# Optimization experiments

Measured on AMD Instinct MI355X. Metric: run time of the kernel, lower is better.

Reference implementation:

```python
import jax, jax.numpy as jnp
import numpy as np
from jax import lax

D_MODEL = 1024
D_STATE = 16
D_CONV = 4
EXPAND = 2
D_INNER = EXPAND * D_MODEL          # 2048
DT_RANK = (D_MODEL + 15) // 16      # 64


def setup_inputs() -> dict:
    key = jax.random.key(0)
    ks = jax.random.split(key, 12)
    B, L = 2, 2048
    s = lambda *sh: 1.0 / np.sqrt(sh[-1])
    inp = {
        "x": jax.random.normal(ks[0], (B, L, D_MODEL), jnp.float32),
        "in_proj_w": jax.random.normal(ks[1], (2 * D_INNER, D_MODEL), jnp.float32) * s(0, D_MODEL),
        "conv_w": jax.random.normal(ks[2], (D_INNER, 1, D_CONV), jnp.float32) * s(0, D_CONV),
        "conv_b": jax.random.normal(ks[3], (D_INNER,), jnp.float32) * 0.01,
        "x_proj_w": jax.random.normal(ks[4], (DT_RANK + 2 * D_STATE, D_INNER), jnp.float32) * s(0, D_INNER),
        "dt_proj_w": jax.random.normal(ks[5], (D_INNER, DT_RANK), jnp.float32) * s(0, DT_RANK),
        "dt_proj_b": jax.random.normal(ks[6], (D_INNER,), jnp.float32) * 0.1 - 4.0,  # softplus(dt) small
        "A_log": jnp.log(jnp.broadcast_to(jnp.arange(1, D_STATE + 1, dtype=jnp.float32), (D_INNER, D_STATE))),
        "D": jnp.ones((D_INNER,), jnp.float32),
        "out_proj_w": jax.random.normal(ks[7], (D_MODEL, D_INNER), jnp.float32) * s(0, D_INNER),
        "ln_w": jnp.ones((D_MODEL,), jnp.float32),
        "ln_b": jnp.zeros((D_MODEL,), jnp.float32),
    }
    return inp


def _mamba(x, in_proj_w, conv_w, conv_b, x_proj_w, dt_proj_w, dt_proj_b, A_log, D, out_proj_w):
    B, L, _ = x.shape
    xz = jnp.einsum("bld,ed->ble", x, in_proj_w)          # [B,L,2*d_inner]
    xi, z = jnp.split(xz, 2, axis=-1)                       # each [B,L,d_inner]

    # causal depthwise conv1d over time
    xt = jnp.transpose(xi, (0, 2, 1))                       # [B,d_inner,L]
    xc = lax.conv_general_dilated(
        xt, conv_w, window_strides=(1,), padding=[(D_CONV - 1, 0)],
        dimension_numbers=("NCH", "OIH", "NCH"), feature_group_count=D_INNER)
    xc = jax.nn.silu(xc + conv_b[None, :, None])            # [B,d_inner,L]
    u = jnp.transpose(xc, (0, 2, 1))                        # [B,L,d_inner]

    x_dbl = jnp.einsum("bld,ed->ble", u, x_proj_w)          # [B,L,dt_rank+2N]
    dt, Bm, Cm = jnp.split(x_dbl, [DT_RANK, DT_RANK + D_STATE], axis=-1)
    delta = jax.nn.softplus(jnp.einsum("blr,dr->bld", dt, dt_proj_w) + dt_proj_b)  # [B,L,d_inner]

    A = -jnp.exp(A_log)                                     # [d_inner,N]

    def step(h, inputs):
        d_t, B_t, C_t, u_t = inputs                         # [B,d], [B,N], [B,N], [B,d]
        dA = jnp.exp(d_t[..., None] * A)                    # [B,d_inner,N]
        h = dA * h + (d_t * u_t)[..., None] * B_t[:, None, :]
        y_t = jnp.einsum("bdn,bn->bd", h, C_t)
        return h, y_t

    xs = (jnp.transpose(delta, (1, 0, 2)), jnp.transpose(Bm, (1, 0, 2)),
          jnp.transpose(Cm, (1, 0, 2)), jnp.transpose(u, (1, 0, 2)))
    h0 = jnp.zeros((B, D_INNER, D_STATE), x.dtype)
    _, ys = lax.scan(step, h0, xs)                          # ys [L,B,d_inner]
    y = jnp.transpose(ys, (1, 0, 2)) + u * D                # skip connection
    y = y * jax.nn.silu(z)                                  # gate
    return jnp.einsum("bld,ed->ble", y, out_proj_w)         # [B,L,d_model]


def reference(x, in_proj_w, conv_w, conv_b, x_proj_w, dt_proj_w, dt_proj_b,
              A_log, D, out_proj_w, ln_w, ln_b):
    residual = x
    y = _mamba(x, in_proj_w, conv_w, conv_b, x_proj_w, dt_proj_w, dt_proj_b,
               A_log, D, out_proj_w)
    # dropout is identity in eval; residual + LayerNorm
    h = y + residual
    mu = jnp.mean(h, axis=-1, keepdims=True)
    var = jnp.var(h, axis=-1, keepdims=True)
    return (h - mu) * lax.rsqrt(var + 1e-5) * ln_w + ln_b
```

## Files before the change

kernel.cpp:

```cpp
#include <hip/hip_runtime.h>

typedef unsigned short u16;
typedef __attribute__((ext_vector_type(8))) short bf8_t;
typedef __attribute__((ext_vector_type(4))) float f4_t;
typedef __attribute__((ext_vector_type(4))) unsigned short u16x4;
typedef __attribute__((ext_vector_type(8))) unsigned short u16x8;

__device__ __forceinline__ float b2f(u16 h) {
  union { unsigned u; float f; } v; v.u = ((unsigned)h) << 16; return v.f;
}
__device__ __forceinline__ u16 f2b(float f) {
  union { float f; unsigned u; } v; v.f = f;
  unsigned u = v.u;
  u += 0x7fffu + ((u >> 16) & 1u);
  return (u16)(u >> 16);
}

#define AS1C(p) ((const __attribute__((address_space(1))) void*)(p))
#define AS3(p)  ((__attribute__((address_space(3))) void*)(p))

__global__ __launch_bounds__(256)
void cvt_all(const float* __restrict__ x, const float* __restrict__ inW,
             const float* __restrict__ xprojW, const float* __restrict__ dtW,
             const float* __restrict__ outW,
             u16* __restrict__ xb, u16* __restrict__ inWb, u16* __restrict__ xpb,
             u16* __restrict__ dtWb, u16* __restrict__ outWb)
{
  int i = blockIdx.x * 256 + threadIdx.x;
  if (i >= 2703360) return;
  const float* s; u16* d; int off;
  if (i < 1048576)      { s = x;      d = xb;    off = i; }
  else if (i < 2097152) { s = inW;    d = inWb;  off = i - 1048576; }
  else if (i < 2146304) { s = xprojW; d = xpb;   off = i - 2097152; }
  else if (i < 2179072) { s = dtW;    d = dtWb;  off = i - 2146304; }
  else                  { s = outW;   d = outWb; off = i - 2179072; }
  f4_t v = *(const f4_t*)(s + (size_t)off * 4);
  u16x4 o;
#pragma unroll
  for (int j = 0; j < 4; ++j) o[j] = f2b(v[j]);
  *(u16x4*)(d + (size_t)off * 4) = o;
}

__device__ __forceinline__ void stage64(const u16* g, int ld, int row0, int rowmax,
                                        int k0, u16* lds, int wid, int lane) {
  int qg = (lane & 7) ^ ((lane >> 3) & 7);
#pragma unroll
  for (int c = 0; c < 4; ++c) {
    int chunk = wid * 4 + c;
    int r = row0 + chunk * 8 + (lane >> 3);
    if (r > rowmax) r = rowmax;
    const u16* gp = g + (size_t)r * ld + k0 + qg * 8;
    __builtin_amdgcn_global_load_lds(AS1C(gp), AS3(lds + chunk * 512), 16, 0, 0);
  }
}

template<int EPI>
__device__ __forceinline__ void gemm_body(const u16* __restrict__ A, int lda,
             const u16* __restrict__ Bt, int ldb,
             int Kblk, int Nact,
             u16* __restrict__ o16, float* __restrict__ of32,
             float* __restrict__ of32b, const float* __restrict__ biasf)
{
  __shared__ u16 lsA[128 * 64];
  __shared__ u16 lsB[128 * 64];
  const int tid = threadIdx.x;
  const int wid = tid >> 6, lane = tid & 63;
  const int wm = wid >> 1, wn = wid & 1;
  const int lrow = lane & 15;
  const int kq = lane >> 4;
  const int sw = lrow & 7;
  const int m0 = blockIdx.y * 128;
  const int n0 = (EPI == 1) ? 0 : blockIdx.x * 128;
  int kbase = 0;
  if (EPI == 1) kbase = blockIdx.x * Kblk;

  f4_t acc[4][4];
#pragma unroll
  for (int i = 0; i < 4; ++i)
#pragma unroll
    for (int j = 0; j < 4; ++j) acc[i][j] = {0.f, 0.f, 0.f, 0.f};

  for (int kt = kbase; kt < kbase + Kblk; kt += 64) {
    stage64(A,  lda, m0, 0x3fffffff, kt, lsA, wid, lane);
    stage64(Bt, ldb, n0, Nact - 1,   kt, lsB, wid, lane);
    __syncthreads();
#pragma unroll
    for (int h = 0; h < 2; ++h) {
      const int lk = ((h * 4 + kq) ^ sw) * 8;
      bf8_t af[4], bfr[4];
#pragma unroll
      for (int mi = 0; mi < 4; ++mi)
        af[mi] = *(const bf8_t*)&lsA[(wm * 64 + mi * 16 + lrow) * 64 + lk];
#pragma unroll
      for (int ni = 0; ni < 4; ++ni)
        bfr[ni] = *(const bf8_t*)&lsB[(wn * 64 + ni * 16 + lrow) * 64 + lk];
#pragma unroll
      for (int mi = 0; mi < 4; ++mi)
#pragma unroll
        for (int ni = 0; ni < 4; ++ni)
          acc[mi][ni] = __builtin_amdgcn_mfma_f32_16x16x32_bf16(af[mi], bfr[ni], acc[mi][ni], 0, 0, 0);
    }
    __syncthreads();
  }

  const int rq = (lane >> 4) * 4;
#pragma unroll
  for (int mi = 0; mi < 4; ++mi) {
#pragma unroll
    for (int ni = 0; ni < 4; ++ni) {
#pragma unroll
      for (int r = 0; r < 4; ++r) {
        int m = m0 + wm * 64 + mi * 16 + rq + r;
        int n = n0 + wn * 64 + ni * 16 + lrow;
        float v = acc[mi][ni][r];
        if (EPI == 1) {
          if (n < 96) of32[((size_t)blockIdx.x * 4096 + m) * 96 + n] = v;
        } else if (EPI == 2) {
          float t = v + biasf[n];
          float sp = (t > 20.f) ? t : log1pf(__expf(t));
          o16[(size_t)m * 2048 + n] = f2b(sp);
        }
      }
    }
  }
}

__global__ __launch_bounds__(256)
void gemm_xp(const u16* A, int lda, const u16* Bt, int ldb, int Kblk, int Nact,
             u16* o16, float* of32, float* of32b, const float* biasf)
{ gemm_body<1>(A, lda, Bt, ldb, Kblk, Nact, o16, of32, of32b, biasf); }

__global__ __launch_bounds__(256)
void gemm_dt(const u16* A, int lda, const u16* Bt, int ldb, int Kblk, int Nact,
             u16* o16, float* of32, float* of32b, const float* biasf)
{ gemm_body<2>(A, lda, Bt, ldb, Kblk, Nact, o16, of32, of32b, biasf); }


__device__ __forceinline__ void stageu(const u16* __restrict__ g, int ld,
                                       int row0, int k0, u16* ldsu,
                                       int wid, int lane) {
  int qg = (lane & 7) ^ ((lane >> 3) & 7);
#pragma unroll
  for (int j = 0; j < 2; ++j) {
    int rr = j * 64 + wid * 8 + (lane >> 3);
    const u16* gp = g + (size_t)(row0 + rr) * ld + k0 + qg * 8;
    __builtin_amdgcn_global_load_lds(AS1C(gp), AS3(ldsu + (j * 512 + wid * 64) * 8), 16, 0, 0);
  }
}

#define G8_BAR()   __builtin_amdgcn_s_barrier()
#define G8_LGKM0() do { asm volatile("s_waitcnt lgkmcnt(0)" ::: "memory"); \
                        __builtin_amdgcn_sched_barrier(0); } while (0)
#define G8_LGKM8() asm volatile("s_waitcnt lgkmcnt(8)" ::: "memory")
#define G8_VM(N)   do { asm volatile("s_waitcnt vmcnt(" #N ")" ::: "memory"); \
                        __builtin_amdgcn_sched_barrier(0); } while (0)

#define RD_A(base, MH) do { \
  _Pragma("unroll") \
  for (int mi_ = 0; mi_ < 4; ++mi_) { \
    af[mi_][0] = *(const bf8_t*)((base) + arow + ((MH) * 64 + mi_ * 16) * 64 + aq0); \
    af[mi_][1] = *(const bf8_t*)((base) + arow + ((MH) * 64 + mi_ * 16) * 64 + aq1); \
  } } while (0)

#define RD_B(base, NH) do { \
  _Pragma("unroll") \
  for (int ni_ = 0; ni_ < 2; ++ni_) { \
    bfr[NH][ni_][0] = *(const bf8_t*)((base) + brow + ((NH) * 32 + ni_ * 16) * 64 + aq0); \
    bfr[NH][ni_][1] = *(const bf8_t*)((base) + brow + ((NH) * 32 + ni_ * 16) * 64 + aq1); \
  } } while (0)

#define MMA(MH, NH) do { \
  __builtin_amdgcn_s_setprio(1); \
  _Pragma("unroll") \
  for (int mi_ = 0; mi_ < 4; ++mi_) \
    _Pragma("unroll") \
    for (int ni_ = 0; ni_ < 2; ++ni_) { \
      acc[(MH) * 4 + mi_][(NH) * 2 + ni_] = __builtin_amdgcn_mfma_f32_16x16x32_bf16( \
          af[mi_][0], bfr[NH][ni_][0], acc[(MH) * 4 + mi_][(NH) * 2 + ni_], 0, 0, 0); \
      acc[(MH) * 4 + mi_][(NH) * 2 + ni_] = __builtin_amdgcn_mfma_f32_16x16x32_bf16( \
          af[mi_][1], bfr[NH][ni_][1], acc[(MH) * 4 + mi_][(NH) * 2 + ni_], 0, 0, 0); \
    } \
  __builtin_amdgcn_s_setprio(0); \
} while (0)

__global__ __launch_bounds__(512, 2)
void gemm8_in(const u16* __restrict__ A, const u16* __restrict__ Bt,
              u16* __restrict__ o16)
{
  __shared__ u16 ls[65536];
  const int tid = threadIdx.x;
  const int wid = tid >> 6, lane = tid & 63;
  const int wm = wid >> 2, wn = wid & 3;
  const int lrow = lane & 15;
  const int kq = lane >> 4;
  const int sw = lrow & 7;
  const int m0 = blockIdx.y * 256;
  const int n0 = blockIdx.x * 256;
  u16* lsA0 = ls;
  u16* lsB0 = ls + 16384;
  u16* lsA1 = ls + 32768;
  u16* lsB1 = ls + 49152;
  const int arow = (wm * 128 + lrow) * 64;
  const int brow = (wn * 64 + lrow) * 64;
  const int aq0 = (kq ^ sw) * 8;
  const int aq1 = ((4 + kq) ^ sw) * 8;

  f4_t acc[8][4];
#pragma unroll
  for (int i = 0; i < 8; ++i)
#pragma unroll
    for (int j = 0; j < 4; ++j) acc[i][j] = {0.f, 0.f, 0.f, 0.f};
  bf8_t af[4][2];
  bf8_t bfr[2][2][2];

  stageu(A,  1024, m0,        0, lsA0,        wid, lane);
  stageu(A,  1024, m0 + 128,  0, lsA0 + 8192, wid, lane);
  stageu(Bt, 1024, n0,        0, lsB0,        wid, lane);
  stageu(Bt, 1024, n0 + 128,  0, lsB0 + 8192, wid, lane);
  stageu(Bt, 1024, n0,       64, lsB1,        wid, lane);
  stageu(Bt, 1024, n0 + 128, 64, lsB1 + 8192, wid, lane);
  G8_VM(4); G8_BAR();

#pragma unroll 1
  for (int i = 0; i < 7; ++i) {
    const int k1 = (2 * i + 1) * 64, k2 = k1 + 64, k3 = k1 + 128;
    RD_A(lsA0, 0); RD_B(lsB0, 0);
    stageu(A, 1024, m0, k1, lsA1, wid, lane);
    G8_LGKM8(); G8_BAR(); G8_LGKM0(); MMA(0, 0); G8_BAR();
    RD_B(lsB0, 1);
    stageu(A, 1024, m0 + 128, k1, lsA1 + 8192, wid, lane);
    G8_BAR(); G8_LGKM0(); MMA(0, 1); G8_BAR();
    RD_A(lsA0, 1);
    stageu(Bt, 1024, n0, k2, lsB0, wid, lane);
    G8_BAR(); G8_LGKM0(); MMA(1, 0); G8_BAR();
    stageu(Bt, 1024, n0 + 128, k2, lsB0 + 8192, wid, lane);
    G8_BAR(); G8_LGKM0(); MMA(1, 1); G8_VM(4); G8_BAR();
    RD_A(lsA1, 0); RD_B(lsB1, 0);
    stageu(A, 1024, m0, k2, lsA0, wid, lane);
    G8_LGKM8(); G8_BAR(); G8_LGKM0(); MMA(0, 0); G8_BAR();
    RD_B(lsB1, 1);
    stageu(A, 1024, m0 + 128, k2, lsA0 + 8192, wid, lane);
    G8_BAR(); G8_LGKM0(); MMA(0, 1); G8_BAR();
    RD_A(lsA1, 1);
    stageu(Bt, 1024, n0, k3, lsB1, wid, lane);
    G8_BAR(); G8_LGKM0(); MMA(1, 0); G8_BAR();
    stageu(Bt, 1024, n0 + 128, k3, lsB1 + 8192, wid, lane);
    G8_BAR(); G8_LGKM0(); MMA(1, 1); G8_VM(4); G8_BAR();
  }

  {
    const int k1 = 960;
    RD_A(lsA0, 0); RD_B(lsB0, 0);
    stageu(A, 1024, m0, k1, lsA1, wid, lane);
    G8_LGKM8(); G8_BAR(); G8_LGKM0(); MMA(0, 0); G8_BAR();
    RD_B(lsB0, 1);
    stageu(A, 1024, m0 + 128, k1, lsA1 + 8192, wid, lane);
    G8_BAR(); G8_LGKM0(); MMA(0, 1); G8_BAR();
    RD_A(lsA0, 1);
    G8_BAR(); G8_LGKM0(); MMA(1, 0); G8_BAR();
    G8_BAR(); G8_LGKM0(); MMA(1, 1); G8_VM(0); G8_BAR();
    RD_A(lsA1, 0); RD_B(lsB1, 0);
    G8_BAR(); G8_LGKM0(); MMA(0, 0); G8_BAR();
    RD_B(lsB1, 1);
    G8_BAR(); G8_LGKM0(); MMA(0, 1); G8_BAR();
    RD_A(lsA1, 1);
    G8_BAR(); G8_LGKM0(); MMA(1, 0); G8_BAR();
    G8_LGKM0(); MMA(1, 1);
  }

  const int rq = (lane >> 4) * 4;
#pragma unroll
  for (int mi = 0; mi < 8; ++mi) {
#pragma unroll
    for (int ni = 0; ni < 4; ++ni) {
#pragma unroll
      for (int r = 0; r < 4; ++r) {
        int m = m0 + wm * 128 + mi * 16 + rq + r;
        int n = n0 + wn * 64 + ni * 16 + lrow;
        float v = acc[mi][ni][r];
        if (n < 2048) o16[(size_t)m * 2048 + n] = f2b(v);
        else          o16[(size_t)8388608 + (size_t)m * 2048 + (n - 2048)] = f2b(v);
      }
    }
  }
}


#define ORD_A(base, MH) do { \
  _Pragma("unroll") \
  for (int mi_ = 0; mi_ < 2; ++mi_) { \
    af[mi_][0] = *(const bf8_t*)((base) + arow + ((MH) * 32 + mi_ * 16) * 64 + aq0); \
    af[mi_][1] = *(const bf8_t*)((base) + arow + ((MH) * 32 + mi_ * 16) * 64 + aq1); \
  } } while (0)

#define OMMA(MH, NH) do { \
  __builtin_amdgcn_s_setprio(1); \
  _Pragma("unroll") \
  for (int mi_ = 0; mi_ < 2; ++mi_) \
    _Pragma("unroll") \
    for (int ni_ = 0; ni_ < 2; ++ni_) { \
      acc[(MH) * 2 + mi_][(NH) * 2 + ni_] = __builtin_amdgcn_mfma_f32_16x16x32_bf16( \
          af[mi_][0], bfr[NH][ni_][0], acc[(MH) * 2 + mi_][(NH) * 2 + ni_], 0, 0, 0); \
      acc[(MH) * 2 + mi_][(NH) * 2 + ni_] = __builtin_amdgcn_mfma_f32_16x16x32_bf16( \
          af[mi_][1], bfr[NH][ni_][1], acc[(MH) * 2 + mi_][(NH) * 2 + ni_], 0, 0, 0); \
    } \
  __builtin_amdgcn_s_setprio(0); \
} while (0)

__global__ __launch_bounds__(512, 2)
void gemm8_out(const u16* __restrict__ A, const u16* __restrict__ Bt,
               float* __restrict__ of32, float* __restrict__ of32b)
{
  __shared__ u16 ls[49152];
  const int tid = threadIdx.x;
  const int wid = tid >> 6, lane = tid & 63;
  const int wm = wid >> 2, wn = wid & 3;
  const int lrow = lane & 15;
  const int kq = lane >> 4;
  const int sw = lrow & 7;
  const int m0 = blockIdx.y * 128;
  const int n0 = blockIdx.x * 256;
  const int kbase = blockIdx.z * 1024;
  u16* lsA0 = ls;
  u16* lsB0 = ls + 8192;
  u16* lsA1 = ls + 24576;
  u16* lsB1 = ls + 32768;
  const int arow = (wm * 64 + lrow) * 64;
  const int brow = (wn >> 1) * 8192 + ((wn & 1) * 64 + lrow) * 64;
  const int aq0 = (kq ^ sw) * 8;
  const int aq1 = ((4 + kq) ^ sw) * 8;

  f4_t acc[4][4];
#pragma unroll
  for (int i = 0; i < 4; ++i)
#pragma unroll
    for (int j = 0; j < 4; ++j) acc[i][j] = {0.f, 0.f, 0.f, 0.f};
  bf8_t af[2][2];
  bf8_t bfr[2][2][2];

  stageu(A,  2048, m0,        kbase,      lsA0,        wid, lane);
  stageu(Bt, 2048, n0,        kbase,      lsB0,        wid, lane);
  stageu(Bt, 2048, n0 + 128,  kbase,      lsB0 + 8192, wid, lane);
  stageu(Bt, 2048, n0,        kbase + 64, lsB1,        wid, lane);
  stageu(Bt, 2048, n0 + 128,  kbase + 64, lsB1 + 8192, wid, lane);
  G8_VM(4); G8_BAR();

#pragma unroll 1
  for (int i = 0; i < 7; ++i) {
    const int k1 = kbase + (2 * i + 1) * 64, k2 = k1 + 64, k3 = k1 + 128;
    ORD_A(lsA0, 0); RD_B(lsB0, 0);
    stageu(A, 2048, m0, k1, lsA1, wid, lane);
    G8_BAR(); G8_LGKM0(); OMMA(0, 0); G8_BAR();
    RD_B(lsB0, 1);
    G8_BAR(); G8_LGKM0(); OMMA(0, 1); G8_BAR();
    ORD_A(lsA0, 1);
    stageu(Bt, 2048, n0, k2, lsB0, wid, lane);
    G8_BAR(); G8_LGKM0(); OMMA(1, 0); G8_BAR();
    stageu(Bt, 2048, n0 + 128, k2, lsB0 + 8192, wid, lane);
    G8_BAR(); G8_LGKM0(); OMMA(1, 1); G8_VM(4); G8_BAR();
    ORD_A(lsA1, 0); RD_B(lsB1, 0);
    stageu(A, 2048, m0, k2, lsA0, wid, lane);
    G8_BAR(); G8_LGKM0(); OMMA(0, 0); G8_BAR();
    RD_B(lsB1, 1);
    G8_BAR(); G8_LGKM0(); OMMA(0, 1); G8_BAR();
    ORD_A(lsA1, 1);
    stageu(Bt, 2048, n0, k3, lsB1, wid, lane);
    G8_BAR(); G8_LGKM0(); OMMA(1, 0); G8_BAR();
    stageu(Bt, 2048, n0 + 128, k3, lsB1 + 8192, wid, lane);
    G8_BAR(); G8_LGKM0(); OMMA(1, 1); G8_VM(4); G8_BAR();
  }

  {
    const int k1 = kbase + 960;
    ORD_A(lsA0, 0); RD_B(lsB0, 0);
    stageu(A, 2048, m0, k1, lsA1, wid, lane);
    G8_BAR(); G8_LGKM0(); OMMA(0, 0); G8_BAR();
    RD_B(lsB0, 1);
    G8_BAR(); G8_LGKM0(); OMMA(0, 1); G8_BAR();
    ORD_A(lsA0, 1);
    G8_BAR(); G8_LGKM0(); OMMA(1, 0); G8_BAR();
    G8_BAR(); G8_LGKM0(); OMMA(1, 1); G8_VM(0); G8_BAR();
    ORD_A(lsA1, 0); RD_B(lsB1, 0);
    G8_BAR(); G8_LGKM0(); OMMA(0, 0); G8_BAR();
    RD_B(lsB1, 1);
    G8_BAR(); G8_LGKM0(); OMMA(0, 1); G8_BAR();
    ORD_A(lsA1, 1);
    G8_BAR(); G8_LGKM0(); OMMA(1, 0); G8_BAR();
    G8_LGKM0(); OMMA(1, 1);
  }

  float* dst = blockIdx.z ? of32b : of32;
  const int rq = (lane >> 4) * 4;
#pragma unroll
  for (int mi = 0; mi < 4; ++mi) {
#pragma unroll
    for (int ni = 0; ni < 4; ++ni) {
#pragma unroll
      for (int r = 0; r < 4; ++r) {
        int m = m0 + wm * 64 + mi * 16 + rq + r;
        int n = n0 + wn * 64 + ni * 16 + lrow;
        dst[(size_t)m * 1024 + n] = acc[mi][ni][r];
      }
    }
  }
}

__global__ __launch_bounds__(256)
void xproj_reduce(const float* __restrict__ part, u16* __restrict__ dtA,
                  float* __restrict__ bc)
{
  int idx = blockIdx.x * 256 + threadIdx.x;
  int m = idx / 96, n = idx - m * 96;
  float s = 0.f;
#pragma unroll
  for (int p = 0; p < 8; ++p) s += part[(size_t)p * 393216 + idx];
  if (n < 64) dtA[(size_t)m * 64 + n] = f2b(s);
  else        bc[(size_t)m * 32 + (n - 64)] = s;
}

__global__ __launch_bounds__(256)
void conv_silu(const u16* __restrict__ xib, const float* __restrict__ cw,
               const float* __restrict__ cb, u16* __restrict__ ub)
{
  int i = blockIdx.x * 256 + threadIdx.x;
  int c8 = (i & 255) * 8;
  int row = i >> 8;
  int l = row & 2047;
  const u16* base = xib + (size_t)row * 2048 + c8;
  u16x8 x0 = {0,0,0,0,0,0,0,0}, x1 = x0, x2 = x0, x3;
  x3 = *(const u16x8*)(base);
  if (l >= 1) x2 = *(const u16x8*)(base - 2048);
  if (l >= 2) x1 = *(const u16x8*)(base - 2 * 2048);
  if (l >= 3) x0 = *(const u16x8*)(base - 3 * 2048);
  f4_t cb0 = *(const f4_t*)(cb + c8);
  f4_t cb1 = *(const f4_t*)(cb + c8 + 4);
  u16x8 o;
#pragma unroll
  for (int j = 0; j < 8; ++j) {
    f4_t w = *(const f4_t*)(cw + (size_t)(c8 + j) * 4);
    float a = (j < 4 ? cb0[j] : cb1[j - 4])
            + w[0] * b2f(x0[j]) + w[1] * b2f(x1[j])
            + w[2] * b2f(x2[j]) + w[3] * b2f(x3[j]);
    float s = a / (1.f + __expf(-a));
    o[j] = f2b(s);
  }
  *(u16x8*)(ub + (size_t)row * 2048 + c8) = o;
}

__global__ __launch_bounds__(256)
void scan_s1(const u16* __restrict__ delta_bf, const u16* __restrict__ ub,
             const float* __restrict__ bc, const float* __restrict__ alog,
             u16* __restrict__ S, float* __restrict__ Q)
{
  int blk = blockIdx.x;
  int g = blk & 7, c = (blk >> 3) & 63, b = blk >> 9;
  int d = g * 256 + threadIdx.x;
  float Av[16];
#pragma unroll
  for (int nq = 0; nq < 4; ++nq) {
    f4_t al = *(const f4_t*)(alog + (size_t)d * 16 + nq * 4);
#pragma unroll
    for (int j = 0; j < 4; ++j) Av[nq * 4 + j] = -__expf(al[j]);
  }
  float Av0 = Av[0];
  bool st = true;
#pragma unroll
  for (int n = 1; n < 16; ++n)
    st = st && (fabsf(Av[n] - (float)(n + 1) * Av0) <= 1e-3f * (float)(n + 1));
  f4_t Qr[4];
#pragma unroll
  for (int nq = 0; nq < 4; ++nq) Qr[nq] = {0.f,0.f,0.f,0.f};
  float Sd = 0.f;
  int row0 = b * 2048 + c * 32;
  if (st) {
#pragma unroll 2
    for (int i = 0; i < 32; ++i) {
      size_t row = (size_t)(row0 + i);
      float dlt = b2f(delta_bf[row * 2048 + d]);
      float uv  = b2f(ub[row * 2048 + d]);
      const float* bp = bc + row * 32;
      f4_t Bv[4];
#pragma unroll
      for (int nq = 0; nq < 4; ++nq) Bv[nq] = *(const f4_t*)(bp + nq * 4);
      float du = dlt * uv;
      float e1 = __expf(dlt * Av0);
      float a = e1;
      Sd += dlt;
#pragma unroll
      for (int n = 0; n < 16; ++n) {
        Qr[n >> 2][n & 3] = a * Qr[n >> 2][n & 3] + du * Bv[n >> 2][n & 3];
        a *= e1;
      }
    }
  } else {
#pragma unroll 2
    for (int i = 0; i < 32; ++i) {
      size_t row = (size_t)(row0 + i);
      float dlt = b2f(delta_bf[row * 2048 + d]);
      float uv  = b2f(ub[row * 2048 + d]);
      const float* bp = bc + row * 32;
      f4_t Bv[4];
#pragma unroll
      for (int nq = 0; nq < 4; ++nq) Bv[nq] = *(const f4_t*)(bp + nq * 4);
      float du = dlt * uv;
      Sd += dlt;
#pragma unroll
      for (int n = 0; n < 16; ++n) {
        float a = __expf(dlt * Av[n]);
        Qr[n >> 2][n & 3] = a * Qr[n >> 2][n & 3] + du * Bv[n >> 2][n & 3];
      }
    }
  }
  S[(size_t)(b * 64 + c) * 2048 + d] = f2b(Sd);
  size_t o = ((size_t)((b * 64 + c) * 2048 + d)) * 16;
#pragma unroll
  for (int nq = 0; nq < 4; ++nq)
    *(f4_t*)(Q + o + nq * 4) = Qr[nq];
}

__global__ __launch_bounds__(256)
void scan_comb(const u16* __restrict__ S16, float* __restrict__ Q,
               const float* __restrict__ alog)
{
  int idx = blockIdx.x * 256 + threadIdx.x;
  int b = idx >> 15, dn = idx & 32767;
  int d = dn >> 4;
  float Av = -__expf(alog[dn]);
  size_t qbase = (size_t)b * 2097152 + dn;
  size_t sbase = (size_t)b * 131072 + d;
  float H = 0.f;
#pragma unroll
  for (int cg = 0; cg < 4; ++cg) {
    float sv[16], qv[16];
#pragma unroll
    for (int j = 0; j < 16; ++j) {
      int c = cg * 16 + j;
      qv[j] = Q[qbase + (size_t)c * 32768];
      sv[j] = b2f(S16[sbase + (size_t)c * 2048]);
    }
#pragma unroll
    for (int j = 0; j < 16; ++j) {
      int c = cg * 16 + j;
      Q[qbase + (size_t)c * 32768] = H;
      H = __expf(Av * sv[j]) * H + qv[j];
    }
  }
}

__global__ __launch_bounds__(256)
void scan_s3(const u16* __restrict__ delta_bf, const u16* __restrict__ ub,
             const float* __restrict__ bc, const float* __restrict__ alog,
             const float* __restrict__ Q, const float* __restrict__ Dw,
             u16* __restrict__ zy)
{
  int blk = blockIdx.x;
  int g = blk & 7, c = (blk >> 3) & 63, b = blk >> 9;
  int d = g * 256 + threadIdx.x;
  float Av[16];
#pragma unroll
  for (int nq = 0; nq < 4; ++nq) {
    f4_t al = *(const f4_t*)(alog + (size_t)d * 16 + nq * 4);
#pragma unroll
    for (int j = 0; j < 4; ++j) Av[nq * 4 + j] = -__expf(al[j]);
  }
  float Av0 = Av[0];
  bool st = true;
#pragma unroll
  for (int n = 1; n < 16; ++n)
    st = st && (fabsf(Av[n] - (float)(n + 1) * Av0) <= 1e-3f * (float)(n + 1));
  f4_t h4[4];
  size_t o = ((size_t)((b * 64 + c) * 2048 + d)) * 16;
#pragma unroll
  for (int nq = 0; nq < 4; ++nq) h4[nq] = *(const f4_t*)(Q + o + nq * 4);
  float Dv = Dw[d];
  int row0 = b * 2048 + c * 32;
  if (st) {
#pragma unroll 2
    for (int i = 0; i < 32; ++i) {
      size_t row = (size_t)(row0 + i);
      float dlt = b2f(delta_bf[row * 2048 + d]);
      float uv  = b2f(ub[row * 2048 + d]);
      const float* bp = bc + row * 32;
      f4_t Bv[4], Cv[4];
#pragma unroll
      for (int nq = 0; nq < 4; ++nq) { Bv[nq] = *(const f4_t*)(bp + nq * 4); Cv[nq] = *(const f4_t*)(bp + 16 + nq * 4); }
      float du = dlt * uv;
      float e1 = __expf(dlt * Av0);
      float a = e1;
      float y = 0.f;
#pragma unroll
      for (int n = 0; n < 16; ++n) {
        float hn = a * h4[n >> 2][n & 3] + du * Bv[n >> 2][n & 3];
        h4[n >> 2][n & 3] = hn;
        y += hn * Cv[n >> 2][n & 3];
        a *= e1;
      }
      float zv = b2f(zy[row * 2048 + d]);
      float ov = (y + Dv * uv) * (zv / (1.f + __expf(-zv)));
      zy[row * 2048 + d] = f2b(ov);
    }
  } else {
#pragma unroll 2
    for (int i = 0; i < 32; ++i) {
      size_t row = (size_t)(row0 + i);
      float dlt = b2f(delta_bf[row * 2048 + d]);
      float uv  = b2f(ub[row * 2048 + d]);
      const float* bp = bc + row * 32;
      f4_t Bv[4], Cv[4];
#pragma unroll
      for (int nq = 0; nq < 4; ++nq) { Bv[nq] = *(const f4_t*)(bp + nq * 4); Cv[nq] = *(const f4_t*)(bp + 16 + nq * 4); }
      float du = dlt * uv;
      float y = 0.f;
#pragma unroll
      for (int n = 0; n < 16; ++n) {
        float a = __expf(dlt * Av[n]);
        float hn = a * h4[n >> 2][n & 3] + du * Bv[n >> 2][n & 3];
        h4[n >> 2][n & 3] = hn;
        y += hn * Cv[n >> 2][n & 3];
      }
      float zv = b2f(zy[row * 2048 + d]);
      float ov = (y + Dv * uv) * (zv / (1.f + __expf(-zv)));
      zy[row * 2048 + d] = f2b(ov);
    }
  }
}

__global__ __launch_bounds__(256)
void ln_kernel(const float* __restrict__ hp0, const float* __restrict__ hp1,
               const float* __restrict__ xin,
               const float* __restrict__ lnw, const float* __restrict__ lnb,
               float* __restrict__ outp)
{
  __shared__ float ssum[4], ssq[4];
  int row = blockIdx.x, t = threadIdx.x;
  f4_t h0 = *(const f4_t*)(hp0 + (size_t)row * 1024 + t * 4);
  f4_t h1 = *(const f4_t*)(hp1 + (size_t)row * 1024 + t * 4);
  f4_t xv = *(const f4_t*)(xin + (size_t)row * 1024 + t * 4);
  float v[4], s = 0.f, q = 0.f;
#pragma unroll
  for (int j = 0; j < 4; ++j) { v[j] = h0[j] + h1[j] + xv[j]; s += v[j]; q += v[j] * v[j]; }
#pragma unroll
  for (int m = 32; m; m >>= 1) { s += __shfl_xor(s, m, 64); q += __shfl_xor(q, m, 64); }
  int wv = t >> 6;
  if ((t & 63) == 0) { ssum[wv] = s; ssq[wv] = q; }
  __syncthreads();
  s = ssum[0] + ssum[1] + ssum[2] + ssum[3];
  q = ssq[0] + ssq[1] + ssq[2] + ssq[3];
  float mu = s * (1.f / 1024.f);
  float var = q * (1.f / 1024.f) - mu * mu;
  float rs = rsqrtf(var + 1e-5f);
  f4_t o;
#pragma unroll
  for (int j = 0; j < 4; ++j)
    o[j] = (v[j] - mu) * rs * lnw[t * 4 + j] + lnb[t * 4 + j];
  *(f4_t*)(outp + (size_t)row * 1024 + t * 4) = o;
}

extern "C" void kernel_launch(void* const* d_in, const int* in_sizes, int n_in,
                              void* d_out, int out_size, void* d_ws, size_t ws_size,
                              hipStream_t stream)
{
  const float* x      = (const float*)d_in[0];
  const float* inW    = (const float*)d_in[1];
  const float* convW  = (const float*)d_in[2];
  const float* convB  = (const float*)d_in[3];
  const float* xprojW = (const float*)d_in[4];
  const float* dtW    = (const float*)d_in[5];
  const float* dtB    = (const float*)d_in[6];
  const float* alog   = (const float*)d_in[7];
  const float* Dw     = (const float*)d_in[8];
  const float* outW   = (const float*)d_in[9];
  const float* lnw    = (const float*)d_in[10];
  const float* lnb    = (const float*)d_in[11];
  float* out = (float*)d_out;

  char* ws = (char*)d_ws;
  u16*   xiz    = (u16*)(ws);
  u16*   zy     = xiz + 8388608;
  u16*   xb     = (u16*)(ws + 33554432);
  u16*   inWb   = xb + 4194304;
  u16*   u_bf   = (u16*)(ws + 33554432);
  u16*   dtA    = (u16*)(ws + 50331648);
  float* bc     = (float*)(ws + 50855936);
  u16*   xprojWb= (u16*)(ws + 51380224);
  u16*   dtWb   = (u16*)(ws + 51773440);
  u16*   outWb  = (u16*)(ws + 52035584);
  u16*   delta  = xiz;
  float* hpart1 = (float*)(ws);
  float* hpart0 = (float*)d_out;
  float* xpart  = (float*)d_out;
  u16*   Sbuf   = dtA;
  float* Qbuf   = (float*)d_out;

  dim3 blk(256);
  cvt_all<<<10560, blk, 0, stream>>>(x, inW, xprojW, dtW, outW,
                                     xb, inWb, xprojWb, dtWb, outWb);
  gemm8_in<<<dim3(16, 16), dim3(512), 0, stream>>>(xb, inWb, xiz);
  conv_silu<<<4096, blk, 0, stream>>>(xiz, convW, convB, u_bf);
  gemm_xp<<<dim3(8, 32), blk, 0, stream>>>(u_bf, 2048, xprojWb, 2048, 256, 96, nullptr, xpart, nullptr, nullptr);
  xproj_reduce<<<1536, blk, 0, stream>>>(xpart, dtA, bc);
  gemm_dt<<<dim3(16, 32), blk, 0, stream>>>(dtA, 64, dtWb, 64, 64, 2048, delta, nullptr, nullptr, dtB);
  scan_s1<<<1024, blk, 0, stream>>>(delta, u_bf, bc, alog, Sbuf, Qbuf);
  scan_comb<<<256, blk, 0, stream>>>(Sbuf, Qbuf, alog);
  scan_s3<<<1024, blk, 0, stream>>>(delta, u_bf, bc, alog, Qbuf, Dw, zy);
  gemm8_out<<<dim3(4, 32, 2), dim3(512), 0, stream>>>(zy, outWb, hpart0, hpart1);
  ln_kernel<<<4096, blk, 0, stream>>>(hpart0, hpart1, x, lnw, lnb, out);
}
```

Measured before the change: 310.4 us.

## Merge MMA phases in input GEMM and double scan chunk length

The in-projection GEMM main loop now issues both B-half LDS reads and both A-half global stages up front, then runs two MMA blocks per barrier pair. This halves the number of barriers and waitcnt points per K step. Separately, the chunked selective scan uses 64-step chunks instead of 32, halving the block count for the scan stages and the number of chunk states written, read and combined. Fewer chunks means less parallelism, 512 blocks on a large GPU, and a longer serial loop per thread. The merged MMA phases also give the GEMM less load/compute interleaving.

```diff
diff --git a/kernel.cpp b/kernel.cpp
--- a/kernel.cpp
+++ b/kernel.cpp
@@ -151,7 +151,6 @@
 #define G8_BAR()   __builtin_amdgcn_s_barrier()
 #define G8_LGKM0() do { asm volatile("s_waitcnt lgkmcnt(0)" ::: "memory"); \
                         __builtin_amdgcn_sched_barrier(0); } while (0)
-#define G8_LGKM8() asm volatile("s_waitcnt lgkmcnt(8)" ::: "memory")
 #define G8_VM(N)   do { asm volatile("s_waitcnt vmcnt(" #N ")" ::: "memory"); \
                         __builtin_amdgcn_sched_barrier(0); } while (0)
 
@@ -223,49 +222,39 @@
 
 #pragma unroll 1
   for (int i = 0; i < 7; ++i) {
-    const int k1 = (2 * i + 1) * 64, k2 = k1 + 64, k3 = k1 + 128;
-    RD_A(lsA0, 0); RD_B(lsB0, 0);
-    stageu(A, 1024, m0, k1, lsA1, wid, lane);
-    G8_LGKM8(); G8_BAR(); G8_LGKM0(); MMA(0, 0); G8_BAR();
-    RD_B(lsB0, 1);
-    stageu(A, 1024, m0 + 128, k1, lsA1 + 8192, wid, lane);
-    G8_BAR(); G8_LGKM0(); MMA(0, 1); G8_BAR();
+    const int ka1 = (2 * i + 1) * 64;
+    const int k2  = ka1 + 64;
+    const int kb3 = ka1 + 128;
+    RD_A(lsA0, 0); RD_B(lsB0, 0); RD_B(lsB0, 1);
+    stageu(A, 1024, m0,       ka1, lsA1,        wid, lane);
+    stageu(A, 1024, m0 + 128, ka1, lsA1 + 8192, wid, lane);
+    G8_BAR(); G8_LGKM0(); MMA(0, 0); MMA(0, 1); G8_BAR();
     RD_A(lsA0, 1);
-    stageu(Bt, 1024, n0, k2, lsB0, wid, lane);
-    G8_BAR(); G8_LGKM0(); MMA(1, 0); G8_BAR();
+    stageu(Bt, 1024, n0,       k2, lsB0,        wid, lane);
     stageu(Bt, 1024, n0 + 128, k2, lsB0 + 8192, wid, lane);
-    G8_BAR(); G8_LGKM0(); MMA(1, 1); G8_VM(4); G8_BAR();
-    RD_A(lsA1, 0); RD_B(lsB1, 0);
-    stageu(A, 1024, m0, k2, lsA0, wid, lane);
-    G8_LGKM8(); G8_BAR(); G8_LGKM0(); MMA(0, 0); G8_BAR();
-    RD_B(lsB1, 1);
+    G8_BAR(); G8_LGKM0(); MMA(1, 0); MMA(1, 1); G8_VM(4); G8_BAR();
+    RD_A(lsA1, 0); RD_B(lsB1, 0); RD_B(lsB1, 1);
+    stageu(A, 1024, m0,       k2, lsA0,        wid, lane);
     stageu(A, 1024, m0 + 128, k2, lsA0 + 8192, wid, lane);
-    G8_BAR(); G8_LGKM0(); MMA(0, 1); G8_BAR();
+    G8_BAR(); G8_LGKM0(); MMA(0, 0); MMA(0, 1); G8_BAR();
     RD_A(lsA1, 1);
-    stageu(Bt, 1024, n0, k3, lsB1, wid, lane);
-    G8_BAR(); G8_LGKM0(); MMA(1, 0); G8_BAR();
-    stageu(Bt, 1024, n0 + 128, k3, lsB1 + 8192, wid, lane);
-    G8_BAR(); G8_LGKM0(); MMA(1, 1); G8_VM(4); G8_BAR();
+    stageu(Bt, 1024, n0,       kb3, lsB1,        wid, lane);
+    stageu(Bt, 1024, n0 + 128, kb3, lsB1 + 8192, wid, lane);
+    G8_BAR(); G8_LGKM0(); MMA(1, 0); MMA(1, 1); G8_VM(4); G8_BAR();
   }
 
   {
-    const int k1 = 960;
-    RD_A(lsA0, 0); RD_B(lsB0, 0);
-    stageu(A, 1024, m0, k1, lsA1, wid, lane);
-    G8_LGKM8(); G8_BAR(); G8_LGKM0(); MMA(0, 0); G8_BAR();
-    RD_B(lsB0, 1);
-    stageu(A, 1024, m0 + 128, k1, lsA1 + 8192, wid, lane);
-    G8_BAR(); G8_LGKM0(); MMA(0, 1); G8_BAR();
+    const int ka1 = 960;
+    RD_A(lsA0, 0); RD_B(lsB0, 0); RD_B(lsB0, 1);
+    stageu(A, 1024, m0,       ka1, lsA1,        wid, lane);
+    stageu(A, 1024, m0 + 128, ka1, lsA1 + 8192, wid, lane);
+    G8_BAR(); G8_LGKM0(); MMA(0, 0); MMA(0, 1); G8_BAR();
     RD_A(lsA0, 1);
-    G8_BAR(); G8_LGKM0(); MMA(1, 0); G8_BAR();
-    G8_BAR(); G8_LGKM0(); MMA(1, 1); G8_VM(0); G8_BAR();
-    RD_A(lsA1, 0); RD_B(lsB1, 0);
-    G8_BAR(); G8_LGKM0(); MMA(0, 0); G8_BAR();
-    RD_B(lsB1, 1);
-    G8_BAR(); G8_LGKM0(); MMA(0, 1); G8_BAR();
+    G8_BAR(); G8_LGKM0(); MMA(1, 0); MMA(1, 1); G8_VM(0); G8_BAR();
+    RD_A(lsA1, 0); RD_B(lsB1, 0); RD_B(lsB1, 1);
+    G8_BAR(); G8_LGKM0(); MMA(0, 0); MMA(0, 1); G8_BAR();
     RD_A(lsA1, 1);
-    G8_BAR(); G8_LGKM0(); MMA(1, 0); G8_BAR();
-    G8_LGKM0(); MMA(1, 1);
+    G8_LGKM0(); MMA(1, 0); MMA(1, 1);
   }
 
   const int rq = (lane >> 4) * 4;
@@ -453,7 +442,7 @@
              u16* __restrict__ S, float* __restrict__ Q)
 {
   int blk = blockIdx.x;
-  int g = blk & 7, c = (blk >> 3) & 63, b = blk >> 9;
+  int g = blk & 7, c = (blk >> 3) & 31, b = blk >> 8;
   int d = g * 256 + threadIdx.x;
   float Av[16];
 #pragma unroll
@@ -471,10 +460,10 @@
 #pragma unroll
   for (int nq = 0; nq < 4; ++nq) Qr[nq] = {0.f,0.f,0.f,0.f};
   float Sd = 0.f;
-  int row0 = b * 2048 + c * 32;
+  int row0 = b * 2048 + c * 64;
   if (st) {
 #pragma unroll 2
-    for (int i = 0; i < 32; ++i) {
+    for (int i = 0; i < 64; ++i) {
       size_t row = (size_t)(row0 + i);
       float dlt = b2f(delta_bf[row * 2048 + d]);
       float uv  = b2f(ub[row * 2048 + d]);
@@ -494,7 +483,7 @@
     }
   } else {
 #pragma unroll 2
-    for (int i = 0; i < 32; ++i) {
+    for (int i = 0; i < 64; ++i) {
       size_t row = (size_t)(row0 + i);
       float dlt = b2f(delta_bf[row * 2048 + d]);
       float uv  = b2f(ub[row * 2048 + d]);
@@ -511,8 +500,8 @@
       }
     }
   }
-  S[(size_t)(b * 64 + c) * 2048 + d] = f2b(Sd);
-  size_t o = ((size_t)((b * 64 + c) * 2048 + d)) * 16;
+  S[(size_t)(b * 32 + c) * 2048 + d] = f2b(Sd);
+  size_t o = ((size_t)((b * 32 + c) * 2048 + d)) * 16;
 #pragma unroll
   for (int nq = 0; nq < 4; ++nq)
     *(f4_t*)(Q + o + nq * 4) = Qr[nq];
@@ -526,11 +515,11 @@
   int b = idx >> 15, dn = idx & 32767;
   int d = dn >> 4;
   float Av = -__expf(alog[dn]);
-  size_t qbase = (size_t)b * 2097152 + dn;
-  size_t sbase = (size_t)b * 131072 + d;
+  size_t qbase = (size_t)b * 1048576 + dn;
+  size_t sbase = (size_t)b * 65536 + d;
   float H = 0.f;
 #pragma unroll
-  for (int cg = 0; cg < 4; ++cg) {
+  for (int cg = 0; cg < 2; ++cg) {
     float sv[16], qv[16];
 #pragma unroll
     for (int j = 0; j < 16; ++j) {
@@ -554,7 +543,7 @@
              u16* __restrict__ zy)
 {
   int blk = blockIdx.x;
-  int g = blk & 7, c = (blk >> 3) & 63, b = blk >> 9;
+  int g = blk & 7, c = (blk >> 3) & 31, b = blk >> 8;
   int d = g * 256 + threadIdx.x;
   float Av[16];
 #pragma unroll
@@ -569,14 +558,14 @@
   for (int n = 1; n < 16; ++n)
     st = st && (fabsf(Av[n] - (float)(n + 1) * Av0) <= 1e-3f * (float)(n + 1));
   f4_t h4[4];
-  size_t o = ((size_t)((b * 64 + c) * 2048 + d)) * 16;
+  size_t o = ((size_t)((b * 32 + c) * 2048 + d)) * 16;
 #pragma unroll
   for (int nq = 0; nq < 4; ++nq) h4[nq] = *(const f4_t*)(Q + o + nq * 4);
   float Dv = Dw[d];
-  int row0 = b * 2048 + c * 32;
+  int row0 = b * 2048 + c * 64;
   if (st) {
 #pragma unroll 2
-    for (int i = 0; i < 32; ++i) {
+    for (int i = 0; i < 64; ++i) {
       size_t row = (size_t)(row0 + i);
       float dlt = b2f(delta_bf[row * 2048 + d]);
       float uv  = b2f(ub[row * 2048 + d]);
@@ -601,7 +590,7 @@
     }
   } else {
 #pragma unroll 2
-    for (int i = 0; i < 32; ++i) {
+    for (int i = 0; i < 64; ++i) {
       size_t row = (size_t)(row0 + i);
       float dlt = b2f(delta_bf[row * 2048 + d]);
       float uv  = b2f(ub[row * 2048 + d]);
@@ -700,9 +689,9 @@
   gemm_xp<<<dim3(8, 32), blk, 0, stream>>>(u_bf, 2048, xprojWb, 2048, 256, 96, nullptr, xpart, nullptr, nullptr);
   xproj_reduce<<<1536, blk, 0, stream>>>(xpart, dtA, bc);
   gemm_dt<<<dim3(16, 32), blk, 0, stream>>>(dtA, 64, dtWb, 64, 64, 2048, delta, nullptr, nullptr, dtB);
-  scan_s1<<<1024, blk, 0, stream>>>(delta, u_bf, bc, alog, Sbuf, Qbuf);
+  scan_s1<<<512, blk, 0, stream>>>(delta, u_bf, bc, alog, Sbuf, Qbuf);
   scan_comb<<<256, blk, 0, stream>>>(Sbuf, Qbuf, alog);
-  scan_s3<<<1024, blk, 0, stream>>>(delta, u_bf, bc, alog, Qbuf, Dw, zy);
+  scan_s3<<<512, blk, 0, stream>>>(delta, u_bf, bc, alog, Qbuf, Dw, zy);
   gemm8_out<<<dim3(4, 32, 2), dim3(512), 0, stream>>>(zy, outWb, hpart0, hpart1);
   ln_kernel<<<4096, blk, 0, stream>>>(hpart0, hpart1, x, lnw, lnb, out);
 }
```

New measurement: 316.7 us. 2.0% more time.
